# Performance work log

Measured on AMD Instinct MI355X. Metric: run time of the kernel, lower is better.

The kernel has to match this reference:

```python
import jax, jax.numpy as jnp
import numpy as np

N_NODES = 100000
N_EDGES = 400000
N_GRAPHS = 2500
DIM = 128
F_IN = 78
N_LAYERS = 3
BN_EPS = 1e-5


def setup_inputs() -> dict:
    key = jax.random.key(0)
    ks = jax.random.split(key, 24)
    def lin(k, fi, fo):
        return jax.random.normal(k, (fi, fo), jnp.float32) / np.sqrt(fi)
    inp = {
        "x": jax.random.normal(ks[0], (N_NODES, F_IN), jnp.float32),
        "edge_index": jax.random.randint(ks[1], (2, N_EDGES), 0, N_NODES, jnp.int32),
        "batch": jnp.sort(jax.random.randint(ks[2], (N_NODES,), 0, N_GRAPHS, jnp.int32)),
        "num_graphs": N_GRAPHS,
        "gcn1_W": lin(ks[3], F_IN, DIM), "gcn1_b": jnp.zeros((DIM,), jnp.float32),
        "gcn2_W": lin(ks[4], DIM, DIM), "gcn2_b": jnp.zeros((DIM,), jnp.float32),
        "gin0_w1": lin(ks[5], F_IN, DIM), "gin0_b1": jnp.zeros((DIM,), jnp.float32),
        "gin0_w2": lin(ks[6], DIM, DIM), "gin0_b2": jnp.zeros((DIM,), jnp.float32),
        # layers 1..2 stacked (same 128->128 shapes)
        "gin_w1": jnp.stack([lin(ks[7], DIM, DIM), lin(ks[8], DIM, DIM)]),
        "gin_b1": jnp.zeros((2, DIM), jnp.float32),
        "gin_w2": jnp.stack([lin(ks[9], DIM, DIM), lin(ks[10], DIM, DIM)]),
        "gin_b2": jnp.zeros((2, DIM), jnp.float32),
        "bn_gamma": jnp.ones((N_LAYERS, DIM), jnp.float32),
        "bn_beta": jnp.zeros((N_LAYERS, DIM), jnp.float32),
    }
    return inp


def reference(x, edge_index, batch, num_graphs,
              gcn1_W, gcn1_b, gcn2_W, gcn2_b,
              gin0_w1, gin0_b1, gin0_w2, gin0_b2,
              gin_w1, gin_b1, gin_w2, gin_b2,
              bn_gamma, bn_beta):
    n = x.shape[0]
    src, dst = edge_index[0], edge_index[1]

    def gcn(h, W, b):
        # linear -> symmetric-normalized aggregation with self loops (PyG GCNConv)
        h = h @ W
        loop = jnp.arange(n, dtype=src.dtype)
        s = jnp.concatenate([src, loop])
        d = jnp.concatenate([dst, loop])
        deg = jax.ops.segment_sum(jnp.ones(s.shape[0], h.dtype), d, num_segments=n)
        dis = jax.lax.rsqrt(deg)  # deg >= 1 thanks to self loops
        norm = (dis[s] * dis[d])[:, None]
        return jax.ops.segment_sum(h[s] * norm, d, num_segments=n) + b

    def gin(h, w1, b1, w2, b2):
        # GINConv, eps=0: mlp(x + sum_{j->i} x_j)
        agg = jax.ops.segment_sum(h[src], dst, num_segments=n)
        z = jax.nn.relu((h + agg) @ w1 + b1)
        return z @ w2 + b2

    def bn(h, g, bt):
        mu = h.mean(0)
        var = ((h - mu) ** 2).mean(0)
        return (h - mu) * jax.lax.rsqrt(var + BN_EPS) * g + bt

    g1 = jax.nn.relu(gcn(x, gcn1_W, gcn1_b))
    g2 = jax.nn.relu(gcn(g1, gcn2_W, gcn2_b))
    g2a = g2 + g1
    g2m = g2 * g1

    h = x
    xs = []
    m = jnp.float32(1.0)
    e = jnp.float32(0.0)
    for i in range(N_LAYERS):
        if i == 0:
            h = gin(h, gin0_w1, gin0_b1, gin0_w2, gin0_b2)
        else:
            h = gin(h, gin_w1[i - 1], gin_b1[i - 1], gin_w2[i - 1], gin_b2[i - 1])
        h = bn(jax.nn.relu(h), bn_gamma[i], bn_beta[i])
        m = m * h
        e = e + h
        xs.append(h)

    rep = jnp.concatenate(xs + [m, e, g1, g2, g2a, g2m], axis=-1)  # [N, 9*DIM]
    return jax.ops.segment_max(rep, batch, num_segments=num_graphs)
```

## Files before the change

kernel.cpp:

```cpp
#include <hip/hip_runtime.h>
#include <math.h>

#define DIMC 128
#define FINC 78
#define REPW 1152
#define SCAN_TILE 1024

typedef __attribute__((ext_vector_type(8))) short short8x;
typedef __attribute__((ext_vector_type(4))) float f32x4;

__device__ inline float b2f(unsigned short u) {
    union { unsigned int i; float f; } v; v.i = ((unsigned int)u) << 16; return v.f;
}
__device__ inline unsigned short f2b(float f) {
    union { float f; unsigned int i; } v; v.f = f;
    unsigned int r = (v.i + 0x7FFFu + ((v.i >> 16) & 1u)) >> 16;
    return (unsigned short)r;
}


__global__ void k_fill_int(int* __restrict__ p, int v, int n) {
    int i = blockIdx.x * blockDim.x + threadIdx.x;
    if (i < n) p[i] = v;
}

__global__ void k_fill(float* __restrict__ p, float v, int n) {
    int i = blockIdx.x * blockDim.x + threadIdx.x;
    if (i < n) p[i] = v;
}

__global__ void k_count(const int* __restrict__ dst, int* __restrict__ cnt, int E) {
    int e = blockIdx.x * blockDim.x + threadIdx.x;
    if (e < E) atomicAdd(&cnt[dst[e]], 1);
}

__launch_bounds__(256)
__global__ void k_tilesum(const int* __restrict__ cnt, int* __restrict__ tileSum, int N) {
    __shared__ int red[256];
    int base = blockIdx.x * SCAN_TILE;
    int s = 0;
    for (int i = threadIdx.x; i < SCAN_TILE; i += 256) {
        int idx = base + i;
        if (idx < N) s += cnt[idx];
    }
    red[threadIdx.x] = s;
    __syncthreads();
    for (int d = 128; d > 0; d >>= 1) {
        if (threadIdx.x < d) red[threadIdx.x] += red[threadIdx.x + d];
        __syncthreads();
    }
    if (threadIdx.x == 0) tileSum[blockIdx.x] = red[0];
}

__launch_bounds__(256)
__global__ void k_tilescan(const int* __restrict__ tileSum, int* __restrict__ tileOff,
                           int* __restrict__ rowptr, int T, int N) {
    __shared__ int sh[256];
    int t = threadIdx.x;
    int orig = (t < T) ? tileSum[t] : 0;
    sh[t] = orig;
    __syncthreads();
    for (int d = 1; d < 256; d <<= 1) {
        int v = (t >= d) ? sh[t - d] : 0;
        __syncthreads();
        sh[t] += v;
        __syncthreads();
    }
    if (t < T) tileOff[t] = sh[t] - orig;
    if (t == 255) rowptr[N] = sh[255];
}

__launch_bounds__(256)
__global__ void k_tileemit(const int* __restrict__ cnt, const int* __restrict__ tileOff,
                           int* __restrict__ rowptr, int* __restrict__ cursor,
                           float* __restrict__ dis, int N) {
    __shared__ int sh[256];
    int t = threadIdx.x;
    int base = blockIdx.x * SCAN_TILE;
    int idx0 = base + t * 4;
    int v0 = 0, v1 = 0, v2 = 0, v3 = 0;
    if (idx0 + 3 < N) {
        int4 v = *(const int4*)(cnt + idx0);
        v0 = v.x; v1 = v.y; v2 = v.z; v3 = v.w;
    } else {
        if (idx0 + 0 < N) v0 = cnt[idx0 + 0];
        if (idx0 + 1 < N) v1 = cnt[idx0 + 1];
        if (idx0 + 2 < N) v2 = cnt[idx0 + 2];
        if (idx0 + 3 < N) v3 = cnt[idx0 + 3];
    }
    int s0 = v0, s1 = s0 + v1, s2 = s1 + v2, s3 = s2 + v3;
    sh[t] = s3;
    __syncthreads();
    for (int d = 1; d < 256; d <<= 1) {
        int v = (t >= d) ? sh[t - d] : 0;
        __syncthreads();
        sh[t] += v;
        __syncthreads();
    }
    int gbase = tileOff[blockIdx.x] + ((t == 0) ? 0 : sh[t - 1]);
    int ex[4] = {0, s0, s1, s2};
    int vv[4] = {v0, v1, v2, v3};
#pragma unroll
    for (int j = 0; j < 4; ++j) {
        int idx = idx0 + j;
        if (idx < N) {
            int r = gbase + ex[j];
            rowptr[idx] = r;
            cursor[idx] = r;
            dis[idx] = rsqrtf((float)vv[j] + 1.0f);
        }
    }
}

__global__ void k_scatter(const int* __restrict__ src, const int* __restrict__ dst,
                          int* __restrict__ cursor, int* __restrict__ col, int E) {
    int e = blockIdx.x * blockDim.x + threadIdx.x;
    if (e < E) {
        int pos = atomicAdd(&cursor[dst[e]], 1);
        col[pos] = src[e];
    }
}

__global__ void k_bounds(const int* __restrict__ batch, int* __restrict__ start, int N, int G) {
    int g = blockIdx.x * blockDim.x + threadIdx.x;
    if (g <= G) {
        int lo = 0, hi = N;
        while (lo < hi) { int mid = (lo + hi) >> 1; if (batch[mid] < g) lo = mid + 1; else hi = mid; }
        start[g] = lo;
    }
}


__global__ void k_cvt_w(const float* __restrict__ s0, const float* __restrict__ s1,
                        const float* __restrict__ s2, const float* __restrict__ s3,
                        const float* __restrict__ s4, const float* __restrict__ s5,
                        const float* __restrict__ s6, const float* __restrict__ s7,
                        unsigned short* __restrict__ whi, unsigned short* __restrict__ wlo) {
    int my = blockIdx.y;
    const float* src; int Ksrc, KP; size_t dstoff;
    const size_t o96 = (size_t)128 * 96, o128 = (size_t)128 * 128;
    switch (my) {
        case 0: src = s0; Ksrc = 78;  KP = 96;  dstoff = 0; break;
        case 1: src = s1; Ksrc = 78;  KP = 96;  dstoff = o96; break;
        case 2: src = s2; Ksrc = 128; KP = 128; dstoff = 2 * o96; break;
        case 3: src = s3; Ksrc = 128; KP = 128; dstoff = 2 * o96 + o128; break;
        case 4: src = s4; Ksrc = 128; KP = 128; dstoff = 2 * o96 + 2 * o128; break;
        case 5: src = s5; Ksrc = 128; KP = 128; dstoff = 2 * o96 + 3 * o128; break;
        case 6: src = s6; Ksrc = 128; KP = 128; dstoff = 2 * o96 + 4 * o128; break;
        default: src = s7; Ksrc = 128; KP = 128; dstoff = 2 * o96 + 5 * o128; break;
    }
    int i = blockIdx.x * blockDim.x + threadIdx.x;
    if (i < 128 * KP) {
        int n = i / KP, k = i - n * KP;
        float v = (k < Ksrc) ? src[(size_t)k * DIMC + n] : 0.f;
        unsigned short hi = f2b(v);
        unsigned short lo = f2b(v - b2f(hi));
        whi[dstoff + i] = hi;
        wlo[dstoff + i] = lo;
    }
}


template<int KREAL, int KP>
__launch_bounds__(256)
__global__ void k_gemm_mfma3(const float* __restrict__ A,
                             const unsigned short* __restrict__ Whi,
                             const unsigned short* __restrict__ Wlo,
                             const float* __restrict__ bias,
                             const float* __restrict__ rowScale,
                             const float* __restrict__ inScale,
                             const float* __restrict__ inShift,
                             float* __restrict__ statsOut,
                             float* __restrict__ C, int N, int doRelu) {
    __shared__ unsigned short sAhi[128 * 32];
    __shared__ unsigned short sAlo[128 * 32];
    __shared__ unsigned short sBhi[128 * 32];
    __shared__ unsigned short sBlo[128 * 32];
    __shared__ float sStats[256];
    const int tid = threadIdx.x;
    const int row0 = blockIdx.x * 128;

    const int wave = tid >> 6;
    const int lane = tid & 63;
    const int lm = lane & 15, q = lane >> 4;
    const int wr = (wave >> 1) * 64, wc = (wave & 1) * 64;

    f32x4 acc[4][4];
#pragma unroll
    for (int a = 0; a < 4; ++a)
#pragma unroll
        for (int b = 0; b < 4; ++b) acc[a][b] = (f32x4){0.f, 0.f, 0.f, 0.f};

    for (int k0 = 0; k0 < KP; k0 += 32) {
        if (k0) __syncthreads();
        for (int s = tid; s < 512; s += 256) {
            int r = s >> 2, g = s & 3;
            int gr = row0 + r;
            float v[8];
            int kb = k0 + g * 8;
            if (gr < N) {
                if (KREAL % 8 == 0) {
                    float4 u0 = *(const float4*)(A + (size_t)gr * KREAL + kb);
                    float4 u1 = *(const float4*)(A + (size_t)gr * KREAL + kb + 4);
                    v[0] = u0.x; v[1] = u0.y; v[2] = u0.z; v[3] = u0.w;
                    v[4] = u1.x; v[5] = u1.y; v[6] = u1.z; v[7] = u1.w;
                } else {
#pragma unroll
                    for (int j = 0; j < 8; ++j) {
                        int k = kb + j;
                        v[j] = (k < KREAL) ? A[(size_t)gr * KREAL + k] : 0.f;
                    }
                }
                if (inScale) {
#pragma unroll
                    for (int j = 0; j < 8; ++j) {
                        int k = kb + j;
                        v[j] = fmaf(v[j], inScale[k], inShift[k]);
                    }
                }
            } else {
#pragma unroll
                for (int j = 0; j < 8; ++j) v[j] = 0.f;
            }
            unsigned int hi[4], lo[4];
#pragma unroll
            for (int j = 0; j < 4; ++j) {
                unsigned short h0 = f2b(v[2 * j]), h1 = f2b(v[2 * j + 1]);
                unsigned short l0 = f2b(v[2 * j] - b2f(h0)), l1 = f2b(v[2 * j + 1] - b2f(h1));
                hi[j] = (unsigned int)h0 | ((unsigned int)h1 << 16);
                lo[j] = (unsigned int)l0 | ((unsigned int)l1 << 16);
            }
            size_t addr = ((size_t)g * 128 + ((r + g) & 127)) * 8;
            *(uint4*)(sAhi + addr) = make_uint4(hi[0], hi[1], hi[2], hi[3]);
            *(uint4*)(sAlo + addr) = make_uint4(lo[0], lo[1], lo[2], lo[3]);
        }
        for (int s = tid; s < 512; s += 256) {
            int n = s >> 2, g = s & 3;
            size_t gaddr = (size_t)n * KP + k0 + g * 8;
            size_t addr = ((size_t)g * 128 + ((n + g) & 127)) * 8;
            *(uint4*)(sBhi + addr) = *(const uint4*)(Whi + gaddr);
            *(uint4*)(sBlo + addr) = *(const uint4*)(Wlo + gaddr);
        }
        __syncthreads();

        short8x ah[4], al[4], bh[4], bl[4];
#pragma unroll
        for (int rt = 0; rt < 4; ++rt) {
            int m = wr + rt * 16 + lm;
            size_t addr = ((size_t)q * 128 + ((m + q) & 127)) * 8;
            ah[rt] = *(const short8x*)(sAhi + addr);
            al[rt] = *(const short8x*)(sAlo + addr);
        }
#pragma unroll
        for (int ct = 0; ct < 4; ++ct) {
            int n = wc + ct * 16 + lm;
            size_t addr = ((size_t)q * 128 + ((n + q) & 127)) * 8;
            bh[ct] = *(const short8x*)(sBhi + addr);
            bl[ct] = *(const short8x*)(sBlo + addr);
        }
#pragma unroll
        for (int rt = 0; rt < 4; ++rt)
#pragma unroll
            for (int ct = 0; ct < 4; ++ct) {
                acc[rt][ct] = __builtin_amdgcn_mfma_f32_16x16x32_bf16(ah[rt], bh[ct], acc[rt][ct], 0, 0, 0);
                acc[rt][ct] = __builtin_amdgcn_mfma_f32_16x16x32_bf16(ah[rt], bl[ct], acc[rt][ct], 0, 0, 0);
                acc[rt][ct] = __builtin_amdgcn_mfma_f32_16x16x32_bf16(al[rt], bh[ct], acc[rt][ct], 0, 0, 0);
            }
    }

    float cs[4] = {0.f, 0.f, 0.f, 0.f}, cq[4] = {0.f, 0.f, 0.f, 0.f};
#pragma unroll
    for (int rt = 0; rt < 4; ++rt) {
#pragma unroll
        for (int i = 0; i < 4; ++i) {
            int row = wr + rt * 16 + q * 4 + i;
            int gr = row0 + row;
            if (gr < N) {
                float sc = rowScale ? rowScale[gr] : 1.f;
#pragma unroll
                for (int ct = 0; ct < 4; ++ct) {
                    int colg = wc + ct * 16 + lm;
                    float v = acc[rt][ct][i];
                    if (bias) v += bias[colg];
                    if (doRelu) v = fmaxf(v, 0.f);
                    v *= sc;
                    C[(size_t)gr * DIMC + colg] = v;
                    if (statsOut) { cs[ct] += v; cq[ct] = fmaf(v, v, cq[ct]); }
                }
            }
        }
    }
    if (statsOut) {
        sStats[tid] = 0.f;
        __syncthreads();
#pragma unroll
        for (int ct = 0; ct < 4; ++ct) {
            int colg = wc + ct * 16 + lm;
            atomicAdd(&sStats[colg], cs[ct]);
            atomicAdd(&sStats[128 + colg], cq[ct]);
        }
        __syncthreads();
        atomicAdd(&statsOut[tid], sStats[tid]);
    }
}


__global__ void k_bn_coef(const float* __restrict__ bnsum, const float* __restrict__ gamma,
                          const float* __restrict__ beta, float* __restrict__ coef, float invN) {
    int c = threadIdx.x;
    float mu  = bnsum[c] * invN;
    float var = bnsum[128 + c] * invN - mu * mu;
    float inv = rsqrtf(var + 1e-5f);
    float s = gamma[c] * inv;
    coef[c] = s;
    coef[128 + c] = beta[c] - mu * s;
}


__global__ void k_gather_gcn(const float4* __restrict__ t, const int* __restrict__ rowptr,
                             const int* __restrict__ col, const float* __restrict__ dis,
                             const float4* __restrict__ bias, float4* __restrict__ out, int N) {
    int i = blockIdx.x * blockDim.x + threadIdx.x;
    int node = i >> 5, c4 = i & 31;
    if (node >= N) return;
    int s = rowptr[node], e = rowptr[node + 1];
    float4 acc = t[(size_t)node * 32 + c4];
    for (int k = s; k < e; ++k) {
        float4 v = t[(size_t)col[k] * 32 + c4];
        acc.x += v.x; acc.y += v.y; acc.z += v.z; acc.w += v.w;
    }
    float d = dis[node];
    float4 b = bias[c4];
    float4 o;
    o.x = fmaxf(acc.x * d + b.x, 0.f);
    o.y = fmaxf(acc.y * d + b.y, 0.f);
    o.z = fmaxf(acc.z * d + b.z, 0.f);
    o.w = fmaxf(acc.w * d + b.w, 0.f);
    out[(size_t)node * 32 + c4] = o;
}

__global__ void k_gather_gin(const float4* __restrict__ t, const int* __restrict__ rowptr,
                             const int* __restrict__ col, const float4* __restrict__ bias,
                             float4* __restrict__ out, int N) {
    int i = blockIdx.x * blockDim.x + threadIdx.x;
    int node = i >> 5, c4 = i & 31;
    if (node >= N) return;
    int s = rowptr[node], e = rowptr[node + 1];
    float4 acc = t[(size_t)node * 32 + c4];
    for (int k = s; k < e; ++k) {
        float4 v = t[(size_t)col[k] * 32 + c4];
        acc.x += v.x; acc.y += v.y; acc.z += v.z; acc.w += v.w;
    }
    float4 b = bias[c4];
    float4 o;
    o.x = fmaxf(acc.x + b.x, 0.f);
    o.y = fmaxf(acc.y + b.y, 0.f);
    o.z = fmaxf(acc.z + b.z, 0.f);
    o.w = fmaxf(acc.w + b.w, 0.f);
    out[(size_t)node * 32 + c4] = o;
}


__global__ void k_segmax_gin_all(const float* __restrict__ h0, const float* __restrict__ h1,
                                 const float* __restrict__ h2, const float* __restrict__ coef,
                                 const int* __restrict__ start, float* __restrict__ out) {
    int g = blockIdx.x, c = threadIdx.x;
    float s0 = coef[c],       t0 = coef[128 + c];
    float s1 = coef[256 + c], t1 = coef[384 + c];
    float s2 = coef[512 + c], t2 = coef[640 + c];
    int s = start[g], e = start[g + 1];
    float m0 = -INFINITY, m1 = -INFINITY, m2 = -INFINITY, mm = -INFINITY, me = -INFINITY;
    for (int n = s; n < e; ++n) {
        size_t idx = (size_t)n * DIMC + c;
        float a0 = fmaf(h0[idx], s0, t0);
        float a1 = fmaf(h1[idx], s1, t1);
        float a2 = fmaf(h2[idx], s2, t2);
        m0 = fmaxf(m0, a0); m1 = fmaxf(m1, a1); m2 = fmaxf(m2, a2);
        mm = fmaxf(mm, a0 * a1 * a2);
        me = fmaxf(me, a0 + a1 + a2);
    }
    size_t o = (size_t)g * REPW + c;
    out[o]            = m0;
    out[o + 1 * DIMC] = m1;
    out[o + 2 * DIMC] = m2;
    out[o + 3 * DIMC] = mm;
    out[o + 4 * DIMC] = me;
}

__global__ void k_segmax_gcn(const float* __restrict__ G1, const float* __restrict__ G2,
                             const int* __restrict__ start, float* __restrict__ out) {
    int g = blockIdx.x, c = threadIdx.x;
    int s = start[g], e = start[g + 1];
    float m1 = -INFINITY, m2 = -INFINITY, ma = -INFINITY, mm = -INFINITY;
    for (int n = s; n < e; ++n) {
        float a = G1[(size_t)n * DIMC + c], b = G2[(size_t)n * DIMC + c];
        m1 = fmaxf(m1, a); m2 = fmaxf(m2, b);
        ma = fmaxf(ma, a + b); mm = fmaxf(mm, a * b);
    }
    size_t o = (size_t)g * REPW + c;
    out[o + 5 * DIMC] = m1;
    out[o + 6 * DIMC] = m2;
    out[o + 7 * DIMC] = ma;
    out[o + 8 * DIMC] = mm;
}


extern "C" void kernel_launch(void* const* d_in, const int* in_sizes, int n_in,
                              void* d_out, int out_size, void* d_ws, size_t ws_size,
                              hipStream_t stream) {
    const float* x       = (const float*)d_in[0];
    const int*   ei      = (const int*)d_in[1];
    const int*   batch   = (const int*)d_in[2];
    const float* gcn1_W  = (const float*)d_in[4];
    const float* gcn1_b  = (const float*)d_in[5];
    const float* gcn2_W  = (const float*)d_in[6];
    const float* gcn2_b  = (const float*)d_in[7];
    const float* gin0_w1 = (const float*)d_in[8];
    const float* gin0_b1 = (const float*)d_in[9];
    const float* gin0_w2 = (const float*)d_in[10];
    const float* gin0_b2 = (const float*)d_in[11];
    const float* gin_w1  = (const float*)d_in[12];
    const float* gin_b1  = (const float*)d_in[13];
    const float* gin_w2  = (const float*)d_in[14];
    const float* gin_b2  = (const float*)d_in[15];
    const float* bn_g    = (const float*)d_in[16];
    const float* bn_b    = (const float*)d_in[17];
    float* out = (float*)d_out;

    const int N = in_sizes[0] / FINC;
    const int E = in_sizes[1] / 2;
    const int G = out_size / REPW;
    const int* srcv = ei;
    const int* dstv = ei + E;

    char* ws = (char*)d_ws;
    size_t off = 0;
    auto alloc = [&](size_t bytes) { char* p = ws + off; off += (bytes + 255) & ~(size_t)255; return p; };
    int*   cnt     = (int*)alloc(N * 4);
    int*   rowptr  = (int*)alloc((N + 1) * 4);
    int*   cursor  = (int*)alloc(N * 4);
    int*   col     = (int*)alloc(E * 4);
    float* dis     = (float*)alloc(N * 4);
    float* bnsum   = (float*)alloc(768 * 4);
    float* coef    = (float*)alloc(768 * 4);
    int*   start   = (int*)alloc((G + 1) * 4);
    int*   tileSum = (int*)alloc(256 * 4);
    int*   tileOff = (int*)alloc(256 * 4);
    const size_t wtElems = 2 * (size_t)128 * 96 + 6 * (size_t)128 * 128;
    unsigned short* whi = (unsigned short*)alloc(wtElems * 2);
    unsigned short* wlo = (unsigned short*)alloc(wtElems * 2);
    float* bufT    = (float*)alloc((size_t)N * DIMC * 4);
    float* bufZ    = (float*)alloc((size_t)N * DIMC * 4);
    float* h0      = (float*)alloc((size_t)N * DIMC * 4);
    float* h1      = (float*)alloc((size_t)N * DIMC * 4);
    float* h2      = (float*)alloc((size_t)N * DIMC * 4);
    (void)ws_size; (void)n_in;

    const size_t o96 = (size_t)128 * 96, o128 = (size_t)128 * 128;
    const size_t woff[8] = {0, o96, 2 * o96, 2 * o96 + o128, 2 * o96 + 2 * o128,
                            2 * o96 + 3 * o128, 2 * o96 + 4 * o128, 2 * o96 + 5 * o128};

    const int T = 256;
    auto cdiv = [](long a, long b) { return (int)((a + b - 1) / b); };
    const int gemmGrid = cdiv(N, 128);
    const int gatherGrid = cdiv((long)N * 32, T);
    const int nTiles = cdiv(N, SCAN_TILE);
    const float invN = 1.0f / (float)N;

    k_fill_int<<<cdiv(N, T), T, 0, stream>>>(cnt, 0, N);
    k_count<<<cdiv(E, T), T, 0, stream>>>(dstv, cnt, E);
    k_tilesum<<<nTiles, T, 0, stream>>>(cnt, tileSum, N);
    k_tilescan<<<1, T, 0, stream>>>(tileSum, tileOff, rowptr, nTiles, N);
    k_tileemit<<<nTiles, T, 0, stream>>>(cnt, tileOff, rowptr, cursor, dis, N);
    k_scatter<<<cdiv(E, T), T, 0, stream>>>(srcv, dstv, cursor, col, E);
    k_bounds<<<cdiv(G + 1, T), T, 0, stream>>>(batch, start, N, G);
    k_fill<<<3, T, 0, stream>>>(bnsum, 0.f, 768);
    {
        dim3 g(64, 8);
        k_cvt_w<<<g, T, 0, stream>>>(gcn1_W, gin0_w1, gcn2_W, gin0_w2,
                                     gin_w1, gin_w1 + o128, gin_w2, gin_w2 + o128, whi, wlo);
    }

    k_gemm_mfma3<FINC, 96><<<gemmGrid, T, 0, stream>>>(x, whi + woff[0], wlo + woff[0],
                                                       nullptr, dis, nullptr, nullptr, nullptr, bufT, N, 0);
    k_gather_gcn<<<gatherGrid, T, 0, stream>>>((const float4*)bufT, rowptr, col, dis,
                                               (const float4*)gcn1_b, (float4*)bufZ, N);
    k_gemm_mfma3<DIMC, 128><<<gemmGrid, T, 0, stream>>>(bufZ, whi + woff[2], wlo + woff[2],
                                                        nullptr, dis, nullptr, nullptr, nullptr, bufT, N, 0);
    k_gather_gcn<<<gatherGrid, T, 0, stream>>>((const float4*)bufT, rowptr, col, dis,
                                               (const float4*)gcn2_b, (float4*)h0, N);
    k_segmax_gcn<<<G, DIMC, 0, stream>>>(bufZ, h0, start, out);

    const int w1i[3] = {1, 4, 5};
    const int w2i[3] = {3, 6, 7};
    const float* b1s[3] = {gin0_b1, gin_b1, gin_b1 + DIMC};
    const float* b2s[3] = {gin0_b2, gin_b2, gin_b2 + DIMC};
    float* hs[3] = {h0, h1, h2};

    for (int L = 0; L < 3; ++L) {
        if (L == 0)
            k_gemm_mfma3<FINC, 96><<<gemmGrid, T, 0, stream>>>(x, whi + woff[1], wlo + woff[1],
                                                               nullptr, nullptr, nullptr, nullptr, nullptr,
                                                               bufT, N, 0);
        else
            k_gemm_mfma3<DIMC, 128><<<gemmGrid, T, 0, stream>>>(hs[L - 1], whi + woff[w1i[L]], wlo + woff[w1i[L]],
                                                                nullptr, nullptr,
                                                                coef + (L - 1) * 256, coef + (L - 1) * 256 + 128,
                                                                nullptr, bufT, N, 0);
        k_gather_gin<<<gatherGrid, T, 0, stream>>>((const float4*)bufT, rowptr, col,
                                                   (const float4*)b1s[L], (float4*)bufZ, N);
        k_gemm_mfma3<DIMC, 128><<<gemmGrid, T, 0, stream>>>(bufZ, whi + woff[w2i[L]], wlo + woff[w2i[L]],
                                                            b2s[L], nullptr, nullptr, nullptr,
                                                            bnsum + L * 256, hs[L], N, 1);
        k_bn_coef<<<1, DIMC, 0, stream>>>(bnsum + L * 256, bn_g + L * DIMC, bn_b + L * DIMC,
                                          coef + L * 256, invN);
    }

    k_segmax_gin_all<<<G, DIMC, 0, stream>>>(h0, h1, h2, coef, start, out);
}
```

Before: 792.1 us.

## Store activations as packed bf16 hi/lo pairs and stream GEMM tiles via LDS DMA

All intermediate activations are now stored as split bf16 hi/lo arrays produced in GEMM and gather epilogues, so GEMMs no longer convert fp32 to bf16 pairs while loading. The GEMM stages tiles with global_load_lds directly into double-buffered LDS and overlaps the next tile's load with the current tile's MFMAs. BN scale/shift is folded into the next layer's weights and a bias vector. Memory traffic per element stays at 4 bytes, and some padded buffers get reused, such as x packed into H1 storage.

Measured after the change: 844.8 us. 6.7% more time.

```diff
diff --git a/kernel.cpp b/kernel.cpp
--- a/kernel.cpp
+++ b/kernel.cpp
@@ -8,6 +8,9 @@
 
 typedef __attribute__((ext_vector_type(8))) short short8x;
 typedef __attribute__((ext_vector_type(4))) float f32x4;
+typedef unsigned int u32;
+typedef const __attribute__((address_space(1))) u32* gas_u32p;
+typedef __attribute__((address_space(3))) u32* las_u32p;
 
 __device__ inline float b2f(unsigned short u) {
     union { unsigned int i; float f; } v; v.i = ((unsigned int)u) << 16; return v.f;
@@ -16,6 +19,11 @@
     union { float f; unsigned int i; } v; v.f = f;
     unsigned int r = (v.i + 0x7FFFu + ((v.i >> 16) & 1u)) >> 16;
     return (unsigned short)r;
+}
+__device__ inline float upk2(unsigned short h, unsigned short l) { return b2f(h) + b2f(l); }
+
+__device__ __forceinline__ void gld16(const void* g, void* l) {
+    __builtin_amdgcn_global_load_lds((gas_u32p)g, (las_u32p)l, 16, 0, 0);
 }
 
 
@@ -161,29 +169,46 @@
 }
 
 
-template<int KREAL, int KP>
-__launch_bounds__(256)
-__global__ void k_gemm_mfma3(const float* __restrict__ A,
-                             const unsigned short* __restrict__ Whi,
-                             const unsigned short* __restrict__ Wlo,
-                             const float* __restrict__ bias,
-                             const float* __restrict__ rowScale,
-                             const float* __restrict__ inScale,
-                             const float* __restrict__ inShift,
-                             float* __restrict__ statsOut,
-                             float* __restrict__ C, int N, int doRelu) {
-    __shared__ unsigned short sAhi[128 * 32];
-    __shared__ unsigned short sAlo[128 * 32];
-    __shared__ unsigned short sBhi[128 * 32];
-    __shared__ unsigned short sBlo[128 * 32];
-    __shared__ float sStats[256];
+__global__ void k_pack_x(const float* __restrict__ x, unsigned short* __restrict__ xhi,
+                         unsigned short* __restrict__ xlo, int N) {
+    int i = blockIdx.x * blockDim.x + threadIdx.x;
+    int r = i / 24, cc = (i - r * 24) * 4;
+    if (r >= N) return;
+    float v[4];
+#pragma unroll
+    for (int j = 0; j < 4; ++j) { int k = cc + j; v[j] = (k < FINC) ? x[(size_t)r * FINC + k] : 0.f; }
+    unsigned short h[4], l[4];
+#pragma unroll
+    for (int j = 0; j < 4; ++j) { h[j] = f2b(v[j]); l[j] = f2b(v[j] - b2f(h[j])); }
+    *(ushort4*)(xhi + (size_t)r * 96 + cc) = make_ushort4(h[0], h[1], h[2], h[3]);
+    *(ushort4*)(xlo + (size_t)r * 96 + cc) = make_ushort4(l[0], l[1], l[2], l[3]);
+}
+
+
+template<int KP>
+__launch_bounds__(256, 2)
+__global__ void k_gemm_pk(const unsigned short* __restrict__ Ahi, const unsigned short* __restrict__ Alo,
+                          const unsigned short* __restrict__ Bhi, const unsigned short* __restrict__ Blo,
+                          const float* __restrict__ bias, const float* __restrict__ rowScale,
+                          float* __restrict__ statsOut,
+                          unsigned short* __restrict__ Ohi, unsigned short* __restrict__ Olo,
+                          int N, int doRelu) {
+    constexpr int NT = KP / 32;
+    __shared__ unsigned short lds[2][4][4096];
     const int tid = threadIdx.x;
-    const int row0 = blockIdx.x * 128;
-
-    const int wave = tid >> 6;
-    const int lane = tid & 63;
+    const int wave = tid >> 6, lane = tid & 63;
     const int lm = lane & 15, q = lane >> 4;
     const int wr = (wave >> 1) * 64, wc = (wave & 1) * 64;
+    const int row0 = blockIdx.x * 128;
+
+    const int rr = tid & 127;
+    const int g0 = tid >> 7;
+    const int o0 = ((g0 ^ (rr & 3)) << 3);
+    const int o1 = (((2 + g0) ^ (rr & 3)) << 3);
+    const size_t arow = (size_t)(row0 + rr) * KP;
+    const size_t brow = (size_t)rr * KP;
+    const int u0 = tid << 3;
+    const int u1 = (256 + tid) << 3;
 
     f32x4 acc[4][4];
 #pragma unroll
@@ -191,116 +216,109 @@
 #pragma unroll
         for (int b = 0; b < 4; ++b) acc[a][b] = (f32x4){0.f, 0.f, 0.f, 0.f};
 
-    for (int k0 = 0; k0 < KP; k0 += 32) {
-        if (k0) __syncthreads();
-        for (int s = tid; s < 512; s += 256) {
-            int r = s >> 2, g = s & 3;
-            int gr = row0 + r;
-            float v[8];
-            int kb = k0 + g * 8;
-            if (gr < N) {
-                if (KREAL % 8 == 0) {
-                    float4 u0 = *(const float4*)(A + (size_t)gr * KREAL + kb);
-                    float4 u1 = *(const float4*)(A + (size_t)gr * KREAL + kb + 4);
-                    v[0] = u0.x; v[1] = u0.y; v[2] = u0.z; v[3] = u0.w;
-                    v[4] = u1.x; v[5] = u1.y; v[6] = u1.z; v[7] = u1.w;
-                } else {
-#pragma unroll
-                    for (int j = 0; j < 8; ++j) {
-                        int k = kb + j;
-                        v[j] = (k < KREAL) ? A[(size_t)gr * KREAL + k] : 0.f;
-                    }
-                }
-                if (inScale) {
-#pragma unroll
-                    for (int j = 0; j < 8; ++j) {
-                        int k = kb + j;
-                        v[j] = fmaf(v[j], inScale[k], inShift[k]);
-                    }
-                }
-            } else {
-#pragma unroll
-                for (int j = 0; j < 8; ++j) v[j] = 0.f;
+    auto stage = [&](int c, int d) {
+        const int cb = c << 5;
+        gld16(Ahi + arow + cb + o0, &lds[d][0][u0]);
+        gld16(Ahi + arow + cb + o1, &lds[d][0][u1]);
+        gld16(Alo + arow + cb + o0, &lds[d][1][u0]);
+        gld16(Alo + arow + cb + o1, &lds[d][1][u1]);
+        gld16(Bhi + brow + cb + o0, &lds[d][2][u0]);
+        gld16(Bhi + brow + cb + o1, &lds[d][2][u1]);
+        gld16(Blo + brow + cb + o0, &lds[d][3][u0]);
+        gld16(Blo + brow + cb + o1, &lds[d][3][u1]);
+    };
+
+    stage(0, 0);
+#pragma unroll
+    for (int t = 0; t < NT; ++t) {
+        const int cur = t & 1;
+        if (t + 1 < NT) {
+            stage(t + 1, cur ^ 1);
+            asm volatile("s_waitcnt vmcnt(8)" ::: "memory");
+        } else {
+            asm volatile("s_waitcnt vmcnt(0)" ::: "memory");
+        }
+        __builtin_amdgcn_s_barrier();
+        __builtin_amdgcn_sched_barrier(0);
+
+        short8x ah[4], al[4], bh[4], bl[4];
+#pragma unroll
+        for (int yt = 0; yt < 4; ++yt) {
+            int m = wr + yt * 16 + lm;
+            int sl = ((q ^ (m & 3)) * 128 + m) << 3;
+            ah[yt] = *(const short8x*)&lds[cur][0][sl];
+            al[yt] = *(const short8x*)&lds[cur][1][sl];
+        }
+#pragma unroll
+        for (int xt = 0; xt < 4; ++xt) {
+            int n = wc + xt * 16 + lm;
+            int sl = ((q ^ (n & 3)) * 128 + n) << 3;
+            bh[xt] = *(const short8x*)&lds[cur][2][sl];
+            bl[xt] = *(const short8x*)&lds[cur][3][sl];
+        }
+#pragma unroll
+        for (int xt = 0; xt < 4; ++xt)
+#pragma unroll
+            for (int yt = 0; yt < 4; ++yt) {
+                acc[xt][yt] = __builtin_amdgcn_mfma_f32_16x16x32_bf16(bh[xt], ah[yt], acc[xt][yt], 0, 0, 0);
+                acc[xt][yt] = __builtin_amdgcn_mfma_f32_16x16x32_bf16(bh[xt], al[yt], acc[xt][yt], 0, 0, 0);
+                acc[xt][yt] = __builtin_amdgcn_mfma_f32_16x16x32_bf16(bl[xt], ah[yt], acc[xt][yt], 0, 0, 0);
             }
-            unsigned int hi[4], lo[4];
-#pragma unroll
-            for (int j = 0; j < 4; ++j) {
-                unsigned short h0 = f2b(v[2 * j]), h1 = f2b(v[2 * j + 1]);
-                unsigned short l0 = f2b(v[2 * j] - b2f(h0)), l1 = f2b(v[2 * j + 1] - b2f(h1));
-                hi[j] = (unsigned int)h0 | ((unsigned int)h1 << 16);
-                lo[j] = (unsigned int)l0 | ((unsigned int)l1 << 16);
-            }
-            size_t addr = ((size_t)g * 128 + ((r + g) & 127)) * 8;
-            *(uint4*)(sAhi + addr) = make_uint4(hi[0], hi[1], hi[2], hi[3]);
-            *(uint4*)(sAlo + addr) = make_uint4(lo[0], lo[1], lo[2], lo[3]);
-        }
-        for (int s = tid; s < 512; s += 256) {
-            int n = s >> 2, g = s & 3;
-            size_t gaddr = (size_t)n * KP + k0 + g * 8;
-            size_t addr = ((size_t)g * 128 + ((n + g) & 127)) * 8;
-            *(uint4*)(sBhi + addr) = *(const uint4*)(Whi + gaddr);
-            *(uint4*)(sBlo + addr) = *(const uint4*)(Wlo + gaddr);
-        }
-        __syncthreads();
-
-        short8x ah[4], al[4], bh[4], bl[4];
-#pragma unroll
-        for (int rt = 0; rt < 4; ++rt) {
-            int m = wr + rt * 16 + lm;
-            size_t addr = ((size_t)q * 128 + ((m + q) & 127)) * 8;
-            ah[rt] = *(const short8x*)(sAhi + addr);
-            al[rt] = *(const short8x*)(sAlo + addr);
-        }
-#pragma unroll
-        for (int ct = 0; ct < 4; ++ct) {
-            int n = wc + ct * 16 + lm;
-            size_t addr = ((size_t)q * 128 + ((n + q) & 127)) * 8;
-            bh[ct] = *(const short8x*)(sBhi + addr);
-            bl[ct] = *(const short8x*)(sBlo + addr);
-        }
-#pragma unroll
-        for (int rt = 0; rt < 4; ++rt)
-#pragma unroll
-            for (int ct = 0; ct < 4; ++ct) {
-                acc[rt][ct] = __builtin_amdgcn_mfma_f32_16x16x32_bf16(ah[rt], bh[ct], acc[rt][ct], 0, 0, 0);
-                acc[rt][ct] = __builtin_amdgcn_mfma_f32_16x16x32_bf16(ah[rt], bl[ct], acc[rt][ct], 0, 0, 0);
-                acc[rt][ct] = __builtin_amdgcn_mfma_f32_16x16x32_bf16(al[rt], bh[ct], acc[rt][ct], 0, 0, 0);
-            }
-    }
-
-    float cs[4] = {0.f, 0.f, 0.f, 0.f}, cq[4] = {0.f, 0.f, 0.f, 0.f};
-#pragma unroll
-    for (int rt = 0; rt < 4; ++rt) {
-#pragma unroll
-        for (int i = 0; i < 4; ++i) {
-            int row = wr + rt * 16 + q * 4 + i;
-            int gr = row0 + row;
-            if (gr < N) {
-                float sc = rowScale ? rowScale[gr] : 1.f;
-#pragma unroll
-                for (int ct = 0; ct < 4; ++ct) {
-                    int colg = wc + ct * 16 + lm;
-                    float v = acc[rt][ct][i];
-                    if (bias) v += bias[colg];
+        __builtin_amdgcn_s_barrier();
+    }
+
+    float cs[4][4], cq[4][4];
+#pragma unroll
+    for (int xt = 0; xt < 4; ++xt)
+#pragma unroll
+        for (int i = 0; i < 4; ++i) { cs[xt][i] = 0.f; cq[xt][i] = 0.f; }
+
+#pragma unroll
+    for (int yt = 0; yt < 4; ++yt) {
+        int m = wr + yt * 16 + lm;
+        int gr = row0 + m;
+        if (gr < N) {
+            float sc = rowScale ? rowScale[gr] : 1.f;
+#pragma unroll
+            for (int xt = 0; xt < 4; ++xt) {
+                int nb = wc + xt * 16 + q * 4;
+                unsigned short h4[4], l4[4];
+#pragma unroll
+                for (int i = 0; i < 4; ++i) {
+                    float v = acc[xt][yt][i];
+                    if (bias) v += bias[nb + i];
                     if (doRelu) v = fmaxf(v, 0.f);
                     v *= sc;
-                    C[(size_t)gr * DIMC + colg] = v;
-                    if (statsOut) { cs[ct] += v; cq[ct] = fmaf(v, v, cq[ct]); }
+                    cs[xt][i] += v; cq[xt][i] = fmaf(v, v, cq[xt][i]);
+                    h4[i] = f2b(v);
+                    l4[i] = f2b(v - b2f(h4[i]));
+                }
+                *(ushort4*)(Ohi + (size_t)gr * DIMC + nb) = make_ushort4(h4[0], h4[1], h4[2], h4[3]);
+                *(ushort4*)(Olo + (size_t)gr * DIMC + nb) = make_ushort4(l4[0], l4[1], l4[2], l4[3]);
+            }
+        }
+    }
+
+    if (statsOut) {
+        float* sSt = (float*)&lds[0][0][0];
+        __syncthreads();
+        sSt[tid] = 0.f;
+        __syncthreads();
+#pragma unroll
+        for (int xt = 0; xt < 4; ++xt)
+#pragma unroll
+            for (int i = 0; i < 4; ++i) {
+                float vs = cs[xt][i], vq = cq[xt][i];
+#pragma unroll
+                for (int o = 1; o < 16; o <<= 1) { vs += __shfl_xor(vs, o); vq += __shfl_xor(vq, o); }
+                if (lm == 0) {
+                    int nb = wc + xt * 16 + q * 4 + i;
+                    atomicAdd(&sSt[nb], vs);
+                    atomicAdd(&sSt[DIMC + nb], vq);
                 }
             }
-        }
-    }
-    if (statsOut) {
-        sStats[tid] = 0.f;
-        __syncthreads();
-#pragma unroll
-        for (int ct = 0; ct < 4; ++ct) {
-            int colg = wc + ct * 16 + lm;
-            atomicAdd(&sStats[colg], cs[ct]);
-            atomicAdd(&sStats[128 + colg], cq[ct]);
-        }
-        __syncthreads();
-        atomicAdd(&statsOut[tid], sStats[tid]);
+        __syncthreads();
+        atomicAdd(&statsOut[tid], sSt[tid]);
     }
 }
 
@@ -317,53 +335,84 @@
 }
 
 
-__global__ void k_gather_gcn(const float4* __restrict__ t, const int* __restrict__ rowptr,
-                             const int* __restrict__ col, const float* __restrict__ dis,
-                             const float4* __restrict__ bias, float4* __restrict__ out, int N) {
+__global__ void k_fold_w(const float* __restrict__ w1, const float* __restrict__ coefL,
+                         unsigned short* __restrict__ fwhi, unsigned short* __restrict__ fwlo,
+                         float* __restrict__ cvec) {
+    __shared__ float red[128];
+    int n = blockIdx.x, k = threadIdx.x;
+    float w = w1[(size_t)k * DIMC + n];
+    float ws = w * coefL[k];
+    unsigned short h = f2b(ws);
+    fwhi[(size_t)n * DIMC + k] = h;
+    fwlo[(size_t)n * DIMC + k] = f2b(ws - b2f(h));
+    red[k] = w * coefL[DIMC + k];
+    __syncthreads();
+    for (int d = 64; d > 0; d >>= 1) { if (k < d) red[k] += red[k + d]; __syncthreads(); }
+    if (k == 0) cvec[n] = red[0];
+}
+
+
+__global__ void k_gather_gcn_pk(const unsigned short* __restrict__ Thi, const unsigned short* __restrict__ Tlo,
+                                const int* __restrict__ rowptr, const int* __restrict__ col,
+                                const float* __restrict__ dis, const float* __restrict__ bias,
+                                unsigned short* __restrict__ Ohi, unsigned short* __restrict__ Olo, int N) {
     int i = blockIdx.x * blockDim.x + threadIdx.x;
-    int node = i >> 5, c4 = i & 31;
+    int node = i >> 5, cc = (i & 31) << 2;
     if (node >= N) return;
     int s = rowptr[node], e = rowptr[node + 1];
-    float4 acc = t[(size_t)node * 32 + c4];
+    size_t sp = (size_t)node * DIMC + cc;
+    ushort4 h = *(const ushort4*)(Thi + sp), l = *(const ushort4*)(Tlo + sp);
+    float a0 = upk2(h.x, l.x), a1 = upk2(h.y, l.y), a2 = upk2(h.z, l.z), a3 = upk2(h.w, l.w);
     for (int k = s; k < e; ++k) {
-        float4 v = t[(size_t)col[k] * 32 + c4];
-        acc.x += v.x; acc.y += v.y; acc.z += v.z; acc.w += v.w;
+        size_t p = (size_t)col[k] * DIMC + cc;
+        ushort4 hh = *(const ushort4*)(Thi + p), ll = *(const ushort4*)(Tlo + p);
+        a0 += upk2(hh.x, ll.x); a1 += upk2(hh.y, ll.y); a2 += upk2(hh.z, ll.z); a3 += upk2(hh.w, ll.w);
     }
     float d = dis[node];
-    float4 b = bias[c4];
-    float4 o;
-    o.x = fmaxf(acc.x * d + b.x, 0.f);
-    o.y = fmaxf(acc.y * d + b.y, 0.f);
-    o.z = fmaxf(acc.z * d + b.z, 0.f);
-    o.w = fmaxf(acc.w * d + b.w, 0.f);
-    out[(size_t)node * 32 + c4] = o;
-}
-
-__global__ void k_gather_gin(const float4* __restrict__ t, const int* __restrict__ rowptr,
-                             const int* __restrict__ col, const float4* __restrict__ bias,
-                             float4* __restrict__ out, int N) {
+    float4 b = ((const float4*)bias)[i & 31];
+    float v0 = fmaxf(fmaf(a0, d, b.x), 0.f);
+    float v1 = fmaxf(fmaf(a1, d, b.y), 0.f);
+    float v2 = fmaxf(fmaf(a2, d, b.z), 0.f);
+    float v3 = fmaxf(fmaf(a3, d, b.w), 0.f);
+    unsigned short oh[4] = {f2b(v0), f2b(v1), f2b(v2), f2b(v3)};
+    *(ushort4*)(Ohi + sp) = make_ushort4(oh[0], oh[1], oh[2], oh[3]);
+    *(ushort4*)(Olo + sp) = make_ushort4(f2b(v0 - b2f(oh[0])), f2b(v1 - b2f(oh[1])),
+                                         f2b(v2 - b2f(oh[2])), f2b(v3 - b2f(oh[3])));
+}
+
+__global__ void k_gather_gin_pk(const unsigned short* __restrict__ Thi, const unsigned short* __restrict__ Tlo,
+                                const int* __restrict__ rowptr, const int* __restrict__ col,
+                                const float* __restrict__ bias,
+                                unsigned short* __restrict__ Ohi, unsigned short* __restrict__ Olo, int N) {
     int i = blockIdx.x * blockDim.x + threadIdx.x;
-    int node = i >> 5, c4 = i & 31;
+    int node = i >> 5, cc = (i & 31) << 2;
     if (node >= N) return;
     int s = rowptr[node], e = rowptr[node + 1];
-    float4 acc = t[(size_t)node * 32 + c4];
+    size_t sp = (size_t)node * DIMC + cc;
+    ushort4 h = *(const ushort4*)(Thi + sp), l = *(const ushort4*)(Tlo + sp);
+    float a0 = upk2(h.x, l.x), a1 = upk2(h.y, l.y), a2 = upk2(h.z, l.z), a3 = upk2(h.w, l.w);
     for (int k = s; k < e; ++k) {
-        float4 v = t[(size_t)col[k] * 32 + c4];
-        acc.x += v.x; acc.y += v.y; acc.z += v.z; acc.w += v.w;
-    }
-    float4 b = bias[c4];
-    float4 o;
-    o.x = fmaxf(acc.x + b.x, 0.f);
-    o.y = fmaxf(acc.y + b.y, 0.f);
-    o.z = fmaxf(acc.z + b.z, 0.f);
-    o.w = fmaxf(acc.w + b.w, 0.f);
-    out[(size_t)node * 32 + c4] = o;
-}
-
-
-__global__ void k_segmax_gin_all(const float* __restrict__ h0, const float* __restrict__ h1,
-                                 const float* __restrict__ h2, const float* __restrict__ coef,
-                                 const int* __restrict__ start, float* __restrict__ out) {
+        size_t p = (size_t)col[k] * DIMC + cc;
+        ushort4 hh = *(const ushort4*)(Thi + p), ll = *(const ushort4*)(Tlo + p);
+        a0 += upk2(hh.x, ll.x); a1 += upk2(hh.y, ll.y); a2 += upk2(hh.z, ll.z); a3 += upk2(hh.w, ll.w);
+    }
+    float4 b = ((const float4*)bias)[i & 31];
+    float v0 = fmaxf(a0 + b.x, 0.f);
+    float v1 = fmaxf(a1 + b.y, 0.f);
+    float v2 = fmaxf(a2 + b.z, 0.f);
+    float v3 = fmaxf(a3 + b.w, 0.f);
+    unsigned short oh[4] = {f2b(v0), f2b(v1), f2b(v2), f2b(v3)};
+    *(ushort4*)(Ohi + sp) = make_ushort4(oh[0], oh[1], oh[2], oh[3]);
+    *(ushort4*)(Olo + sp) = make_ushort4(f2b(v0 - b2f(oh[0])), f2b(v1 - b2f(oh[1])),
+                                         f2b(v2 - b2f(oh[2])), f2b(v3 - b2f(oh[3])));
+}
+
+
+__global__ void k_segmax_gin_all_pk(const unsigned short* __restrict__ h0h, const unsigned short* __restrict__ h0l,
+                                    const unsigned short* __restrict__ h1h, const unsigned short* __restrict__ h1l,
+                                    const unsigned short* __restrict__ h2h, const unsigned short* __restrict__ h2l,
+                                    const float* __restrict__ coef, const int* __restrict__ start,
+                                    float* __restrict__ out) {
     int g = blockIdx.x, c = threadIdx.x;
     float s0 = coef[c],       t0 = coef[128 + c];
     float s1 = coef[256 + c], t1 = coef[384 + c];
@@ -372,9 +421,9 @@
     float m0 = -INFINITY, m1 = -INFINITY, m2 = -INFINITY, mm = -INFINITY, me = -INFINITY;
     for (int n = s; n < e; ++n) {
         size_t idx = (size_t)n * DIMC + c;
-        float a0 = fmaf(h0[idx], s0, t0);
-        float a1 = fmaf(h1[idx], s1, t1);
-        float a2 = fmaf(h2[idx], s2, t2);
+        float a0 = fmaf(upk2(h0h[idx], h0l[idx]), s0, t0);
+        float a1 = fmaf(upk2(h1h[idx], h1l[idx]), s1, t1);
+        float a2 = fmaf(upk2(h2h[idx], h2l[idx]), s2, t2);
         m0 = fmaxf(m0, a0); m1 = fmaxf(m1, a1); m2 = fmaxf(m2, a2);
         mm = fmaxf(mm, a0 * a1 * a2);
         me = fmaxf(me, a0 + a1 + a2);
@@ -387,13 +436,16 @@
     out[o + 4 * DIMC] = me;
 }
 
-__global__ void k_segmax_gcn(const float* __restrict__ G1, const float* __restrict__ G2,
-                             const int* __restrict__ start, float* __restrict__ out) {
+__global__ void k_segmax_gcn_pk(const unsigned short* __restrict__ g1h, const unsigned short* __restrict__ g1l,
+                                const unsigned short* __restrict__ g2h, const unsigned short* __restrict__ g2l,
+                                const int* __restrict__ start, float* __restrict__ out) {
     int g = blockIdx.x, c = threadIdx.x;
     int s = start[g], e = start[g + 1];
     float m1 = -INFINITY, m2 = -INFINITY, ma = -INFINITY, mm = -INFINITY;
     for (int n = s; n < e; ++n) {
-        float a = G1[(size_t)n * DIMC + c], b = G2[(size_t)n * DIMC + c];
+        size_t idx = (size_t)n * DIMC + c;
+        float a = upk2(g1h[idx], g1l[idx]);
+        float b = upk2(g2h[idx], g2l[idx]);
         m1 = fmaxf(m1, a); m2 = fmaxf(m2, b);
         ma = fmaxf(ma, a + b); mm = fmaxf(mm, a * b);
     }
@@ -430,33 +482,46 @@
     const int N = in_sizes[0] / FINC;
     const int E = in_sizes[1] / 2;
     const int G = out_size / REPW;
+    const int NP = (N + 127) & ~127;
     const int* srcv = ei;
     const int* dstv = ei + E;
 
     char* ws = (char*)d_ws;
     size_t off = 0;
     auto alloc = [&](size_t bytes) { char* p = ws + off; off += (bytes + 255) & ~(size_t)255; return p; };
-    int*   cnt     = (int*)alloc(N * 4);
-    int*   rowptr  = (int*)alloc((N + 1) * 4);
-    int*   cursor  = (int*)alloc(N * 4);
-    int*   col     = (int*)alloc(E * 4);
-    float* dis     = (float*)alloc(N * 4);
+    int*   cnt     = (int*)alloc((size_t)N * 4);
+    int*   rowptr  = (int*)alloc(((size_t)N + 1) * 4);
+    int*   cursor  = (int*)alloc((size_t)N * 4);
+    int*   col     = (int*)alloc((size_t)E * 4);
+    float* dis     = (float*)alloc((size_t)N * 4);
     float* bnsum   = (float*)alloc(768 * 4);
     float* coef    = (float*)alloc(768 * 4);
-    int*   start   = (int*)alloc((G + 1) * 4);
+    float* cvec    = (float*)alloc(128 * 4);
+    int*   start   = (int*)alloc(((size_t)G + 1) * 4);
     int*   tileSum = (int*)alloc(256 * 4);
     int*   tileOff = (int*)alloc(256 * 4);
-    const size_t wtElems = 2 * (size_t)128 * 96 + 6 * (size_t)128 * 128;
-    unsigned short* whi = (unsigned short*)alloc(wtElems * 2);
-    unsigned short* wlo = (unsigned short*)alloc(wtElems * 2);
-    float* bufT    = (float*)alloc((size_t)N * DIMC * 4);
-    float* bufZ    = (float*)alloc((size_t)N * DIMC * 4);
-    float* h0      = (float*)alloc((size_t)N * DIMC * 4);
-    float* h1      = (float*)alloc((size_t)N * DIMC * 4);
-    float* h2      = (float*)alloc((size_t)N * DIMC * 4);
+    const size_t o96 = (size_t)128 * 96, o128 = (size_t)128 * 128;
+    const size_t wtElems = 2 * o96 + 6 * o128;
+    unsigned short* whi  = (unsigned short*)alloc(wtElems * 2);
+    unsigned short* wlo  = (unsigned short*)alloc(wtElems * 2);
+    unsigned short* fwhi = (unsigned short*)alloc(o128 * 2);
+    unsigned short* fwlo = (unsigned short*)alloc(o128 * 2);
+    const size_t pbytesP = (size_t)NP * DIMC * 2;
+    const size_t pbytesN = (size_t)N  * DIMC * 2;
+    unsigned short* Thi = (unsigned short*)alloc(pbytesN);
+    unsigned short* Tlo = (unsigned short*)alloc(pbytesN);
+    unsigned short* Zhi = (unsigned short*)alloc(pbytesP);
+    unsigned short* Zlo = (unsigned short*)alloc(pbytesP);
+    unsigned short* H0h = (unsigned short*)alloc(pbytesP);
+    unsigned short* H0l = (unsigned short*)alloc(pbytesP);
+    unsigned short* H1h = (unsigned short*)alloc(pbytesP);
+    unsigned short* H1l = (unsigned short*)alloc(pbytesP);
+    unsigned short* H2h = (unsigned short*)alloc(pbytesN);
+    unsigned short* H2l = (unsigned short*)alloc(pbytesN);
+    unsigned short* xhi = H1h;
+    unsigned short* xlo = H1l;
     (void)ws_size; (void)n_in;
 
-    const size_t o96 = (size_t)128 * 96, o128 = (size_t)128 * 128;
     const size_t woff[8] = {0, o96, 2 * o96, 2 * o96 + o128, 2 * o96 + 2 * o128,
                             2 * o96 + 3 * o128, 2 * o96 + 4 * o128, 2 * o96 + 5 * o128};
 
@@ -480,41 +545,38 @@
         k_cvt_w<<<g, T, 0, stream>>>(gcn1_W, gin0_w1, gcn2_W, gin0_w2,
                                      gin_w1, gin_w1 + o128, gin_w2, gin_w2 + o128, whi, wlo);
     }
-
-    k_gemm_mfma3<FINC, 96><<<gemmGrid, T, 0, stream>>>(x, whi + woff[0], wlo + woff[0],
-                                                       nullptr, dis, nullptr, nullptr, nullptr, bufT, N, 0);
-    k_gather_gcn<<<gatherGrid, T, 0, stream>>>((const float4*)bufT, rowptr, col, dis,
-                                               (const float4*)gcn1_b, (float4*)bufZ, N);
-    k_gemm_mfma3<DIMC, 128><<<gemmGrid, T, 0, stream>>>(bufZ, whi + woff[2], wlo + woff[2],
-                                                        nullptr, dis, nullptr, nullptr, nullptr, bufT, N, 0);
-    k_gather_gcn<<<gatherGrid, T, 0, stream>>>((const float4*)bufT, rowptr, col, dis,
-                                               (const float4*)gcn2_b, (float4*)h0, N);
-    k_segmax_gcn<<<G, DIMC, 0, stream>>>(bufZ, h0, start, out);
-
-    const int w1i[3] = {1, 4, 5};
-    const int w2i[3] = {3, 6, 7};
-    const float* b1s[3] = {gin0_b1, gin_b1, gin_b1 + DIMC};
-    const float* b2s[3] = {gin0_b2, gin_b2, gin_b2 + DIMC};
-    float* hs[3] = {h0, h1, h2};
-
-    for (int L = 0; L < 3; ++L) {
-        if (L == 0)
-            k_gemm_mfma3<FINC, 96><<<gemmGrid, T, 0, stream>>>(x, whi + woff[1], wlo + woff[1],
-                                                               nullptr, nullptr, nullptr, nullptr, nullptr,
-                                                               bufT, N, 0);
-        else
-            k_gemm_mfma3<DIMC, 128><<<gemmGrid, T, 0, stream>>>(hs[L - 1], whi + woff[w1i[L]], wlo + woff[w1i[L]],
-                                                                nullptr, nullptr,
-                                                                coef + (L - 1) * 256, coef + (L - 1) * 256 + 128,
-                                                                nullptr, bufT, N, 0);
-        k_gather_gin<<<gatherGrid, T, 0, stream>>>((const float4*)bufT, rowptr, col,
-                                                   (const float4*)b1s[L], (float4*)bufZ, N);
-        k_gemm_mfma3<DIMC, 128><<<gemmGrid, T, 0, stream>>>(bufZ, whi + woff[w2i[L]], wlo + woff[w2i[L]],
-                                                            b2s[L], nullptr, nullptr, nullptr,
-                                                            bnsum + L * 256, hs[L], N, 1);
-        k_bn_coef<<<1, DIMC, 0, stream>>>(bnsum + L * 256, bn_g + L * DIMC, bn_b + L * DIMC,
-                                          coef + L * 256, invN);
-    }
-
-    k_segmax_gin_all<<<G, DIMC, 0, stream>>>(h0, h1, h2, coef, start, out);
-}
+    k_pack_x<<<cdiv((long)N * 24, T), T, 0, stream>>>(x, xhi, xlo, N);
+
+    k_gemm_pk<96><<<gemmGrid, T, 0, stream>>>(xhi, xlo, whi + woff[0], wlo + woff[0],
+                                              nullptr, dis, nullptr, Thi, Tlo, N, 0);
+    k_gather_gcn_pk<<<gatherGrid, T, 0, stream>>>(Thi, Tlo, rowptr, col, dis, gcn1_b, Zhi, Zlo, N);
+    k_gemm_pk<128><<<gemmGrid, T, 0, stream>>>(Zhi, Zlo, whi + woff[2], wlo + woff[2],
+                                               nullptr, dis, nullptr, Thi, Tlo, N, 0);
+    k_gather_gcn_pk<<<gatherGrid, T, 0, stream>>>(Thi, Tlo, rowptr, col, dis, gcn2_b, H0h, H0l, N);
+    k_segmax_gcn_pk<<<G, DIMC, 0, stream>>>(Zhi, Zlo, H0h, H0l, start, out);
+
+    k_gemm_pk<96><<<gemmGrid, T, 0, stream>>>(xhi, xlo, whi + woff[1], wlo + woff[1],
+                                              nullptr, nullptr, nullptr, Thi, Tlo, N, 0);
+    k_gather_gin_pk<<<gatherGrid, T, 0, stream>>>(Thi, Tlo, rowptr, col, gin0_b1, Zhi, Zlo, N);
+    k_gemm_pk<128><<<gemmGrid, T, 0, stream>>>(Zhi, Zlo, whi + woff[3], wlo + woff[3],
+                                               gin0_b2, nullptr, bnsum, H0h, H0l, N, 1);
+    k_bn_coef<<<1, DIMC, 0, stream>>>(bnsum, bn_g, bn_b, coef, invN);
+    k_fold_w<<<DIMC, DIMC, 0, stream>>>(gin_w1, coef, fwhi, fwlo, cvec);
+
+    k_gemm_pk<128><<<gemmGrid, T, 0, stream>>>(H0h, H0l, fwhi, fwlo,
+                                               cvec, nullptr, nullptr, Thi, Tlo, N, 0);
+    k_gather_gin_pk<<<gatherGrid, T, 0, stream>>>(Thi, Tlo, rowptr, col, gin_b1, Zhi, Zlo, N);
+    k_gemm_pk<128><<<gemmGrid, T, 0, stream>>>(Zhi, Zlo, whi + woff[6], wlo + woff[6],
+                                               gin_b2, nullptr, bnsum + 256, H1h, H1l, N, 1);
+    k_bn_coef<<<1, DIMC, 0, stream>>>(bnsum + 256, bn_g + DIMC, bn_b + DIMC, coef + 256, invN);
+    k_fold_w<<<DIMC, DIMC, 0, stream>>>(gin_w1 + o128, coef + 256, fwhi, fwlo, cvec);
+
+    k_gemm_pk<128><<<gemmGrid, T, 0, stream>>>(H1h, H1l, fwhi, fwlo,
+                                               cvec, nullptr, nullptr, Thi, Tlo, N, 0);
+    k_gather_gin_pk<<<gatherGrid, T, 0, stream>>>(Thi, Tlo, rowptr, col, gin_b1 + DIMC, Zhi, Zlo, N);
+    k_gemm_pk<128><<<gemmGrid, T, 0, stream>>>(Zhi, Zlo, whi + woff[7], wlo + woff[7],
+                                               gin_b2 + DIMC, nullptr, bnsum + 512, H2h, H2l, N, 1);
+    k_bn_coef<<<1, DIMC, 0, stream>>>(bnsum + 512, bn_g + 2 * DIMC, bn_b + 2 * DIMC, coef + 512, invN);
+
+    k_segmax_gin_all_pk<<<G, DIMC, 0, stream>>>(H0h, H0l, H1h, H1l, H2h, H2l, coef, start, out);
+}
```
